# Kernel optimization log

Hardware: AMD Instinct MI355X
Metric: run time of the kernel (lower is better)

## Reference

```python
import jax, jax.numpy as jnp
import numpy as np

K, D, S, H = 8, 2, 1, 12  # kernel_size, dilation, stride, h_size


def setup_inputs() -> dict:
    key = jax.random.key(0)
    k1, k2 = jax.random.split(key)
    x = jax.random.normal(k1, (32, 2048, 64), dtype=jnp.float32)
    A = jax.random.normal(k2, (64, H, H), dtype=jnp.float32) * 0.1
    return {"x": x, "A": A}


def reference(x, A):
    B, T, C = x.shape
    pad = (K + (K - 1) * (D - 1) - 1) // 2  # = 7
    # replicate padding along time
    xp = jnp.pad(x, ((0, 0), (pad, pad), (0, 0)), mode='edge')  # (B, Tp, C)
    Tp = xp.shape[1]
    seg = (Tp - (K - 1) * D - 1) // S + 1
    # dilated unfold: gather overlapping windows along time
    idx = jnp.arange(seg)[:, None] * S + jnp.arange(K)[None, :] * D  # (seg, K)
    win = xp[:, idx, :]                       # (B, seg, K, C)
    w = win.reshape(B * seg, K, C)            # (N, K, C)
    # path increments within each window
    dx = w[:, 1:, :] - w[:, :-1, :]           # (N, K-1, C)
    # skew-symmetric (so(n)) parametrisation of the Lie-algebra map
    Ask = A - jnp.swapaxes(A, -1, -2)         # (C, H, H)
    M = jnp.einsum('nkc,chw->nkhw', dx, Ask)  # (N, K-1, H, H)
    # matrix exponential of each increment's Lie-algebra element
    E = jax.vmap(jax.scipy.linalg.expm)(M.reshape(-1, H, H)).reshape(M.shape)
    # sequential development: z_{t+1} = z_t @ exp(M_t), z_0 = I
    z0 = jnp.broadcast_to(jnp.eye(H, dtype=x.dtype), (B * seg, H, H))

    def step(z, e):
        return jnp.matmul(z, e), None

    zT, _ = jax.lax.scan(step, z0, jnp.swapaxes(E, 0, 1))  # scan over K-1 steps
    dev = zT.reshape(B, seg, H * H)
    sp = w[:, 0, :].reshape(B, seg, C)        # start point of each partition
    return jnp.concatenate([dev, sp], axis=-1)  # (B, seg, H*H + C)
```

## Files before the change

### kernel.cpp

```cpp
#include <hip/hip_runtime.h>

#define B_ 32
#define T_ 2048
#define C_ 64
#define NP_ 2060
#define MSTRIDE 144

typedef short short8_t __attribute__((ext_vector_type(8)));
typedef float f32x4 __attribute__((ext_vector_type(4)));

__device__ __forceinline__ unsigned short f2bf(float f) {
  unsigned u = __float_as_uint(f);
  return (unsigned short)((u + 0x7FFFu + ((u >> 16) & 1u)) >> 16);
}
__device__ __forceinline__ float bf2f(unsigned short s) {
  return __uint_as_float(((unsigned)s) << 16);
}

__global__ __launch_bounds__(256) void k1_mfma(const float* __restrict__ x,
                                               const float* __restrict__ A,
                                               float* __restrict__ M) {
  __shared__ unsigned int askw[9216];
  const int b = blockIdx.y;
  const int p0 = blockIdx.x * 64;
  const int tid = threadIdx.x;
  const float sc = 1.0f / 16.0f;

  for (int P = tid; P < 4608; P += 256) {
    const int j2 = P & 3;
    const int col = (P >> 2) & 15;
    const int koct = (P >> 6) & 3;
    const int rest = P >> 8;
    const int tile = rest % 9;
    const int ks = rest / 9;
    const int e = tile * 16 + col;
    const int h = e / 12, w = e - h * 12;
    const int c0 = ks * 32 + koct * 8 + j2 * 2;
    const float v0 = (A[c0 * 144 + e] - A[c0 * 144 + w * 12 + h]) * sc;
    const float v1 = (A[(c0 + 1) * 144 + e] - A[(c0 + 1) * 144 + w * 12 + h]) * sc;
    const unsigned short h0 = f2bf(v0), h1 = f2bf(v1);
    const unsigned short l0 = f2bf(v0 - bf2f(h0)), l1 = f2bf(v1 - bf2f(h1));
    const int widx = (((ks * 9 + tile) * 4 + koct) * 16 + col) * 4 + j2;
    askw[widx] = ((unsigned)h1 << 16) | h0;
    askw[4608 + widx] = ((unsigned)l1 << 16) | l0;
  }
  __syncthreads();

  const int wv = tid >> 6;
  const int lane = tid & 63;
  const int mrow = lane & 15;
  const int koct = lane >> 4;
  const int p = p0 + wv * 16 + mrow;
  const int i1 = min(max(p - 7, 0), T_ - 1);
  const int i2 = min(max(p - 5, 0), T_ - 1);
  const float* xb = x + (size_t)b * T_ * C_;

  short8_t ah[2], al[2];
#pragma unroll
  for (int ks = 0; ks < 2; ++ks) {
    const int c0 = ks * 32 + koct * 8;
    const float4 u1a = *(const float4*)(xb + (size_t)i1 * C_ + c0);
    const float4 u1b = *(const float4*)(xb + (size_t)i1 * C_ + c0 + 4);
    const float4 u2a = *(const float4*)(xb + (size_t)i2 * C_ + c0);
    const float4 u2b = *(const float4*)(xb + (size_t)i2 * C_ + c0 + 4);
    float d[8];
    d[0] = u2a.x - u1a.x; d[1] = u2a.y - u1a.y;
    d[2] = u2a.z - u1a.z; d[3] = u2a.w - u1a.w;
    d[4] = u2b.x - u1b.x; d[5] = u2b.y - u1b.y;
    d[6] = u2b.z - u1b.z; d[7] = u2b.w - u1b.w;
#pragma unroll
    for (int j = 0; j < 8; ++j) {
      const unsigned short hs = f2bf(d[j]);
      ah[ks][j] = (short)hs;
      al[ks][j] = (short)f2bf(d[j] - bf2f(hs));
    }
  }

  float* Mb = M + (size_t)b * NP_ * MSTRIDE;
  const int dcol = lane & 15;
  const int pbase = p0 + wv * 16 + (lane >> 4) * 4;
  const char* lds = (const char*)askw;
#pragma unroll
  for (int tile = 0; tile < 9; ++tile) {
    f32x4 acc = {0.f, 0.f, 0.f, 0.f};
#pragma unroll
    for (int ks = 0; ks < 2; ++ks) {
      const int fb = (((ks * 9 + tile) * 4 + koct) * 16 + dcol) * 16;
      const short8_t bh = *(const short8_t*)(lds + fb);
      const short8_t bl = *(const short8_t*)(lds + 18432 + fb);
      acc = __builtin_amdgcn_mfma_f32_16x16x32_bf16(ah[ks], bh, acc, 0, 0, 0);
      acc = __builtin_amdgcn_mfma_f32_16x16x32_bf16(ah[ks], bl, acc, 0, 0, 0);
      acc = __builtin_amdgcn_mfma_f32_16x16x32_bf16(al[ks], bh, acc, 0, 0, 0);
    }
#pragma unroll
    for (int reg = 0; reg < 4; ++reg) {
      const int pr = pbase + reg;
      if (pr < NP_) Mb[(size_t)pr * MSTRIDE + tile * 16 + dcol] = acc[reg];
    }
  }
}

#define QFMAC(C, Bv, Av, O)                                              \
  asm("v_fmac_f32_dpp %0, %1, %2 quad_perm:[" #O "," #O "," #O "," #O    \
      "] row_mask:0xf bank_mask:0xf"                                     \
      : "+v"(C) : "v"(Bv), "v"(Av))
#define QMUL(C, Bv, Av, O)                                               \
  asm("v_mul_f32_dpp %0, %1, %2 quad_perm:[" #O "," #O "," #O "," #O     \
      "] row_mask:0xf bank_mask:0xf"                                     \
      : "=v"(C) : "v"(Bv), "v"(Av))

template <bool ACC>
__device__ __forceinline__ void qmm_t(const float a[3][12], const float b[3][12],
                                      float c[3][12]) {
#define QMM_K(OWNER, E, FIRST)                                           \
  {                                                                      \
    _Pragma("unroll")                                                    \
    for (int i = 0; i < 3; ++i) {                                        \
      const float av = a[i][3 * OWNER + E];                              \
      _Pragma("unroll")                                                  \
      for (int j = 0; j < 12; ++j) {                                     \
        if (FIRST && !ACC) { QMUL(c[i][j], b[E][j], av, OWNER); }        \
        else              { QFMAC(c[i][j], b[E][j], av, OWNER); }        \
      }                                                                  \
    }                                                                    \
  }
  QMM_K(0, 0, true)  QMM_K(0, 1, false) QMM_K(0, 2, false)
  QMM_K(1, 0, false) QMM_K(1, 1, false) QMM_K(1, 2, false)
  QMM_K(2, 0, false) QMM_K(2, 1, false) QMM_K(2, 2, false)
  QMM_K(3, 0, false) QMM_K(3, 1, false) QMM_K(3, 2, false)
#undef QMM_K
}
__device__ __forceinline__ void qmm(const float a[3][12], const float b[3][12],
                                    float c[3][12]) { qmm_t<false>(a, b, c); }
__device__ __forceinline__ void qmma(const float a[3][12], const float b[3][12],
                                     float c[3][12]) { qmm_t<true>(a, b, c); }

__global__ __launch_bounds__(256) void k2_expm(float* __restrict__ M) {
  const int gq = (blockIdx.x * 256 + threadIdx.x) >> 2;
  const int r = threadIdx.x & 3;
  float* gp = M + (size_t)gq * MSTRIDE + 36 * r;

  float a[3][12], t2[3][12], t3[3][12];
#pragma unroll
  for (int i = 0; i < 3; ++i)
#pragma unroll
    for (int q4 = 0; q4 < 3; ++q4) {
      float4 v = *(const float4*)(gp + i * 12 + q4 * 4);
      a[i][q4 * 4 + 0] = v.x;
      a[i][q4 * 4 + 1] = v.y;
      a[i][q4 * 4 + 2] = v.z;
      a[i][q4 * 4 + 3] = v.w;
    }

  qmm(a, a, t2);
  qmm(t2, a, t3);
#pragma unroll
  for (int i = 0; i < 3; ++i)
#pragma unroll
    for (int j = 0; j < 12; ++j) {
      const float av = a[i][j], t2v = t2[i][j], t3v = t3[i][j];
      t2[i][j] = av + t2v * 0.5f + t3v * (1.0f / 6.0f) +
                 ((j == 3 * r + i) ? 1.0f : 0.0f);
      a[i][j] = av * (1.0f / 24.0f) + t2v * (1.0f / 120.0f) +
                t3v * (1.0f / 720.0f);
    }
  qmma(t3, a, t2);

  qmm(t2, t2, t3);
  qmm(t3, t3, t2);
  qmm(t2, t2, t3);
  qmm(t3, t3, t2);

#pragma unroll
  for (int i = 0; i < 3; ++i)
#pragma unroll
    for (int q4 = 0; q4 < 3; ++q4)
      *(float4*)(gp + i * 12 + q4 * 4) =
          make_float4(t2[i][q4 * 4 + 0], t2[i][q4 * 4 + 1],
                      t2[i][q4 * 4 + 2], t2[i][q4 * 4 + 3]);
}

__global__ __launch_bounds__(256) void k3_pair(const float* __restrict__ E,
                                               const float* __restrict__ x,
                                               float* __restrict__ out) {
  const int b = blockIdx.y;
  const int t0 = blockIdx.x * 128;
  const float* Eb = E + (size_t)b * NP_ * MSTRIDE;

  const int r = threadIdx.x & 3;
  const int q = threadIdx.x >> 2;
  const int par = q & 1, jj = q >> 1;
  const int tloc = 4 * jj + par;
  const int t1 = t0 + tloc;

#define LOADB_G(DST, P)                                                  \
  {                                                                      \
    const float* ep = Eb + (size_t)(P) * MSTRIDE + (3 * r) * 12;         \
    _Pragma("unroll")                                                    \
    for (int i = 0; i < 3; ++i) {                                        \
      float4 v0 = *(const float4*)(ep + i * 12 + 0);                     \
      float4 v1 = *(const float4*)(ep + i * 12 + 4);                     \
      float4 v2 = *(const float4*)(ep + i * 12 + 8);                     \
      DST[i][0] = v0.x; DST[i][1] = v0.y; DST[i][2]  = v0.z; DST[i][3]  = v0.w; \
      DST[i][4] = v1.x; DST[i][5] = v1.y; DST[i][6]  = v1.z; DST[i][7]  = v1.w; \
      DST[i][8] = v2.x; DST[i][9] = v2.y; DST[i][10] = v2.z; DST[i][11] = v2.w; \
    }                                                                    \
  }

#define STOREZ(SRCZ, TW)                                                 \
  {                                                                      \
    const size_t obase = ((size_t)b * T_ + (TW)) * 208;                  \
    _Pragma("unroll")                                                    \
    for (int i = 0; i < 3; ++i) {                                        \
      const int row = 3 * r + i;                                         \
      *(float4*)(out + obase + row * 12 + 0) =                           \
          make_float4(SRCZ[i][0], SRCZ[i][1], SRCZ[i][2],  SRCZ[i][3]);  \
      *(float4*)(out + obase + row * 12 + 4) =                           \
          make_float4(SRCZ[i][4], SRCZ[i][5], SRCZ[i][6],  SRCZ[i][7]);  \
      *(float4*)(out + obase + row * 12 + 8) =                           \
          make_float4(SRCZ[i][8], SRCZ[i][9], SRCZ[i][10], SRCZ[i][11]); \
    }                                                                    \
    const int xi = min(max((TW) - 7, 0), T_ - 1);                        \
    const float* xr = x + ((size_t)b * T_ + xi) * C_ + 16 * r;           \
    _Pragma("unroll")                                                    \
    for (int qd = 0; qd < 4; ++qd) {                                     \
      *(float4*)(out + obase + 144 + 16 * r + qd * 4) =                  \
          *(const float4*)(xr + qd * 4);                                 \
    }                                                                    \
  }

  float rr[3][12], cc[3][12], bb[3][12];
  LOADB_G(rr, t1 + 2);
  LOADB_G(bb, t1 + 4);  qmm(rr, bb, cc);
  LOADB_G(bb, t1 + 6);  qmm(cc, bb, rr);
  LOADB_G(bb, t1 + 8);  qmm(rr, bb, cc);
  LOADB_G(bb, t1 + 10); qmm(cc, bb, rr);
  LOADB_G(bb, t1 + 12); qmm(rr, bb, cc);

  LOADB_G(bb, t1);      qmm(bb, cc, rr);
  STOREZ(rr, t1);
  LOADB_G(bb, t1 + 14); qmm(cc, bb, rr);
  STOREZ(rr, t1 + 2);
#undef LOADB_G
#undef STOREZ
}

extern "C" void kernel_launch(void* const* d_in, const int* in_sizes, int n_in,
                              void* d_out, int out_size, void* d_ws, size_t ws_size,
                              hipStream_t stream) {
  (void)in_sizes; (void)n_in; (void)out_size;
  const float* x = (const float*)d_in[0];
  const float* A = (const float*)d_in[1];
  float* out = (float*)d_out;
  float* M = (float*)d_ws;

  const size_t need = (size_t)B_ * NP_ * MSTRIDE * sizeof(float);
  if (ws_size < need) return;

  k1_mfma<<<dim3(33, B_), 256, 0, stream>>>(x, A, M);
  k2_expm<<<dim3((B_ * NP_ * 4) / 256), 256, 0, stream>>>(M);
  k3_pair<<<dim3(T_ / 128, B_), 256, 0, stream>>>(M, x, out);
}
```

Measured before the change: 104.9 us.

## Fuse expm and pairwise chain product into one kernel via LDS

Merges the matrix-exponential kernel and the chained-product kernel. Each block computes the exponentials for its 64 timesteps plus a 12-step halo and keeps them in shared memory, and a subset of threads then does the window products from LDS. This removes the global write and re-read of all exponentials and one kernel launch. In exchange it recomputes halo exponentials (about 19% extra expm work) and leaves most threads idle during the product phase.

```diff
diff --git a/kernel.cpp b/kernel.cpp
--- a/kernel.cpp
+++ b/kernel.cpp
@@ -5,6 +5,7 @@
 #define C_ 64
 #define NP_ 2060
 #define MSTRIDE 144
+#define LSTRIDE 148
 
 typedef short short8_t __attribute__((ext_vector_type(8)));
 typedef float f32x4 __attribute__((ext_vector_type(4)));
@@ -135,67 +136,69 @@
 __device__ __forceinline__ void qmma(const float a[3][12], const float b[3][12],
                                      float c[3][12]) { qmm_t<true>(a, b, c); }
 
-__global__ __launch_bounds__(256) void k2_expm(float* __restrict__ M) {
-  const int gq = (blockIdx.x * 256 + threadIdx.x) >> 2;
-  const int r = threadIdx.x & 3;
-  float* gp = M + (size_t)gq * MSTRIDE + 36 * r;
-
-  float a[3][12], t2[3][12], t3[3][12];
-#pragma unroll
-  for (int i = 0; i < 3; ++i)
-#pragma unroll
-    for (int q4 = 0; q4 < 3; ++q4) {
-      float4 v = *(const float4*)(gp + i * 12 + q4 * 4);
-      a[i][q4 * 4 + 0] = v.x;
-      a[i][q4 * 4 + 1] = v.y;
-      a[i][q4 * 4 + 2] = v.z;
-      a[i][q4 * 4 + 3] = v.w;
-    }
-
-  qmm(a, a, t2);
-  qmm(t2, a, t3);
-#pragma unroll
-  for (int i = 0; i < 3; ++i)
-#pragma unroll
-    for (int j = 0; j < 12; ++j) {
-      const float av = a[i][j], t2v = t2[i][j], t3v = t3[i][j];
-      t2[i][j] = av + t2v * 0.5f + t3v * (1.0f / 6.0f) +
-                 ((j == 3 * r + i) ? 1.0f : 0.0f);
-      a[i][j] = av * (1.0f / 24.0f) + t2v * (1.0f / 120.0f) +
-                t3v * (1.0f / 720.0f);
-    }
-  qmma(t3, a, t2);
-
-  qmm(t2, t2, t3);
-  qmm(t3, t3, t2);
-  qmm(t2, t2, t3);
-  qmm(t3, t3, t2);
-
-#pragma unroll
-  for (int i = 0; i < 3; ++i)
-#pragma unroll
-    for (int q4 = 0; q4 < 3; ++q4)
-      *(float4*)(gp + i * 12 + q4 * 4) =
-          make_float4(t2[i][q4 * 4 + 0], t2[i][q4 * 4 + 1],
-                      t2[i][q4 * 4 + 2], t2[i][q4 * 4 + 3]);
-}
-
-__global__ __launch_bounds__(256) void k3_pair(const float* __restrict__ E,
-                                               const float* __restrict__ x,
-                                               float* __restrict__ out) {
+__global__ __launch_bounds__(320) void k23_fused(const float* __restrict__ M,
+                                                 const float* __restrict__ x,
+                                                 float* __restrict__ out) {
+  __shared__ float eb[76][LSTRIDE];
   const int b = blockIdx.y;
-  const int t0 = blockIdx.x * 128;
-  const float* Eb = E + (size_t)b * NP_ * MSTRIDE;
-
-  const int r = threadIdx.x & 3;
-  const int q = threadIdx.x >> 2;
+  const int t0 = blockIdx.x * 64;
+  const int tid = threadIdx.x;
+  const int q = tid >> 2;
+  const int r = tid & 3;
+
+  if (q < 76) {
+    const int p = t0 + q;
+    const float* gp = M + ((size_t)b * NP_ + p) * MSTRIDE + 36 * r;
+    float a[3][12], t2[3][12], t3[3][12];
+#pragma unroll
+    for (int i = 0; i < 3; ++i)
+#pragma unroll
+      for (int q4 = 0; q4 < 3; ++q4) {
+        float4 v = *(const float4*)(gp + i * 12 + q4 * 4);
+        a[i][q4 * 4 + 0] = v.x;
+        a[i][q4 * 4 + 1] = v.y;
+        a[i][q4 * 4 + 2] = v.z;
+        a[i][q4 * 4 + 3] = v.w;
+      }
+
+    qmm(a, a, t2);
+    qmm(t2, a, t3);
+#pragma unroll
+    for (int i = 0; i < 3; ++i)
+#pragma unroll
+      for (int j = 0; j < 12; ++j) {
+        const float av = a[i][j], t2v = t2[i][j], t3v = t3[i][j];
+        t2[i][j] = av + t2v * 0.5f + t3v * (1.0f / 6.0f) +
+                   ((j == 3 * r + i) ? 1.0f : 0.0f);
+        a[i][j] = av * (1.0f / 24.0f) + t2v * (1.0f / 120.0f) +
+                  t3v * (1.0f / 720.0f);
+      }
+    qmma(t3, a, t2);
+
+    qmm(t2, t2, t3);
+    qmm(t3, t3, t2);
+    qmm(t2, t2, t3);
+    qmm(t3, t3, t2);
+
+    float* lb = &eb[q][0];
+#pragma unroll
+    for (int i = 0; i < 3; ++i) {
+      const int row = 3 * r + i;
+      *(float4*)(lb + row * 12 + 0) = make_float4(t2[i][0], t2[i][1], t2[i][2],  t2[i][3]);
+      *(float4*)(lb + row * 12 + 4) = make_float4(t2[i][4], t2[i][5], t2[i][6],  t2[i][7]);
+      *(float4*)(lb + row * 12 + 8) = make_float4(t2[i][8], t2[i][9], t2[i][10], t2[i][11]);
+    }
+  }
+  __syncthreads();
+
+  if (q >= 32) return;
   const int par = q & 1, jj = q >> 1;
   const int tloc = 4 * jj + par;
   const int t1 = t0 + tloc;
 
-#define LOADB_G(DST, P)                                                  \
+#define LOADB(DST, IDX)                                                  \
   {                                                                      \
-    const float* ep = Eb + (size_t)(P) * MSTRIDE + (3 * r) * 12;         \
+    const float* ep = &eb[(IDX)][(3 * r) * 12];                          \
     _Pragma("unroll")                                                    \
     for (int i = 0; i < 3; ++i) {                                        \
       float4 v0 = *(const float4*)(ep + i * 12 + 0);                     \
@@ -230,18 +233,18 @@
   }
 
   float rr[3][12], cc[3][12], bb[3][12];
-  LOADB_G(rr, t1 + 2);
-  LOADB_G(bb, t1 + 4);  qmm(rr, bb, cc);
-  LOADB_G(bb, t1 + 6);  qmm(cc, bb, rr);
-  LOADB_G(bb, t1 + 8);  qmm(rr, bb, cc);
-  LOADB_G(bb, t1 + 10); qmm(cc, bb, rr);
-  LOADB_G(bb, t1 + 12); qmm(rr, bb, cc);
-
-  LOADB_G(bb, t1);      qmm(bb, cc, rr);
+  LOADB(rr, tloc + 2);
+  LOADB(bb, tloc + 4);  qmm(rr, bb, cc);
+  LOADB(bb, tloc + 6);  qmm(cc, bb, rr);
+  LOADB(bb, tloc + 8);  qmm(rr, bb, cc);
+  LOADB(bb, tloc + 10); qmm(cc, bb, rr);
+  LOADB(bb, tloc + 12); qmm(rr, bb, cc);
+
+  LOADB(bb, tloc);      qmm(bb, cc, rr);
   STOREZ(rr, t1);
-  LOADB_G(bb, t1 + 14); qmm(cc, bb, rr);
+  LOADB(bb, tloc + 14); qmm(cc, bb, rr);
   STOREZ(rr, t1 + 2);
-#undef LOADB_G
+#undef LOADB
 #undef STOREZ
 }
 
@@ -258,6 +261,5 @@
   if (ws_size < need) return;
 
   k1_mfma<<<dim3(33, B_), 256, 0, stream>>>(x, A, M);
-  k2_expm<<<dim3((B_ * NP_ * 4) / 256), 256, 0, stream>>>(M);
-  k3_pair<<<dim3(T_ / 128, B_), 256, 0, stream>>>(M, x, out);
-}
+  k23_fused<<<dim3(T_ / 64, B_), 320, 0, stream>>>(M, x, out);
+}
```

Result: faster. 101.9 us, median of 3 (-2.8%).
